# Kernel optimization log

Hardware: AMD Instinct MI355X
Metric: run time of the kernel (lower is better)

## Reference

```python
import jax, jax.numpy as jnp
import numpy as np

NUM_HEADS = 8
SPLIT_S = 4
DIM = 288            # n_feat * 3 * 3
SCALE = (DIM // NUM_HEADS) ** -0.5  # quirk: uses full dim's head_dim (36), not reduced
EPS = 1e-5


def _extract_patches(x):
    # x: [B,C,H,W] -> [B, C*9, H*W], 3x3 kernel, stride 1, 'same' padding
    B, C, H, W = x.shape
    xp = jnp.pad(x, ((0, 0), (0, 0), (1, 1), (1, 1)))
    pats = jnp.stack([xp[:, :, i:i + H, j:j + W] for i in range(3) for j in range(3)], axis=2)
    return pats.reshape(B, C * 9, H * W)


def _fold(cols, H, W):
    # inverse of extract: [B, C*9, H*W] -> [B,C,H,W], summing overlapping patches
    B, Ck, _ = cols.shape
    C = Ck // 9
    p = cols.reshape(B, C, 3, 3, H, W)
    out = jnp.zeros((B, C, H + 2, W + 2), cols.dtype)
    for i in range(3):
        for j in range(3):
            out = out.at[:, :, i:i + H, j:j + W].add(p[:, :, i, j])
    return out[:, :, 1:H + 1, 1:W + 1]


def _ln(x, w, b):
    mu = x.mean(-1, keepdims=True)
    var = ((x - mu) ** 2).mean(-1, keepdims=True)
    return (x - mu) * jax.lax.rsqrt(var + EPS) * w + b


def _attn(x, reduce_w, qkv_w, proj_w, proj_b):
    # x: [B,N,288] -> reduce -> [B,N,144] -> block-diag attention over s=4 chunks
    x = x @ reduce_w.T
    B, N, C = x.shape
    hd = C // NUM_HEADS
    qkv = (x @ qkv_w.T).reshape(B, N, 3, NUM_HEADS, hd).transpose(2, 0, 3, 1, 4)
    q, k, v = qkv[0], qkv[1], qkv[2]          # [B,h,N,hd]
    chunk = N // SPLIT_S
    q = q.reshape(B, NUM_HEADS, SPLIT_S, chunk, hd)
    k = k.reshape(B, NUM_HEADS, SPLIT_S, chunk, hd)
    v = v.reshape(B, NUM_HEADS, SPLIT_S, chunk, hd)
    attn = jnp.einsum('bhscd,bhsed->bhsce', q, k) * SCALE   # [B,h,s,chunk,chunk]
    attn = jax.nn.softmax(attn, axis=-1)
    out = jnp.einsum('bhsce,bhsed->bhscd', attn, v)          # [B,h,s,chunk,hd]
    out = out.transpose(0, 2, 3, 1, 4).reshape(B, N, C)      # cat chunks on token dim
    return out @ proj_w.T + proj_b


def setup_inputs() -> dict:
    key = jax.random.key(0)
    ks = jax.random.split(key, 12)
    d, dr, dh = DIM, DIM // 2, DIM // 4  # 288, 144, 72
    f = lambda k, shape: (jax.random.normal(k, shape, jnp.float32) * 0.02)
    return {
        'x': jax.random.normal(ks[0], (4, 32, 64, 64), jnp.float32),
        'ln1_w': jnp.ones((d,), jnp.float32), 'ln1_b': jnp.zeros((d,), jnp.float32),
        'reduce_w': f(ks[1], (dr, d)),
        'qkv_w': f(ks[2], (3 * dr, dr)),
        'proj_w': f(ks[3], (d, dr)), 'proj_b': jnp.zeros((d,), jnp.float32),
        'ln2_w': jnp.ones((d,), jnp.float32), 'ln2_b': jnp.zeros((d,), jnp.float32),
        'fc1_w': f(ks[4], (dh, d)), 'fc1_b': jnp.zeros((dh,), jnp.float32),
        'fc2_w': f(ks[5], (d, dh)), 'fc2_b': jnp.zeros((d,), jnp.float32),
    }


def reference(x, ln1_w, ln1_b, reduce_w, qkv_w, proj_w, proj_b, ln2_w, ln2_b, fc1_w, fc1_b, fc2_w, fc2_b):
    B, C, H, W = x.shape
    t = _extract_patches(x).transpose(0, 2, 1)  # [B, N=H*W, 288]
    t = t + _attn(_ln(t, ln1_w, ln1_b), reduce_w, qkv_w, proj_w, proj_b)
    h = _ln(t, ln2_w, ln2_b)
    t = t + (jax.nn.relu(h @ fc1_w.T + fc1_b) @ fc2_w.T + fc2_b)
    return _fold(t.transpose(0, 2, 1), H, W)
```

## Files before the change

kernel.cpp:

```cpp
#include <hip/hip_runtime.h>
#include <hip/hip_bf16.h>

typedef __hip_bfloat16 bf16;
typedef unsigned short u16;
typedef unsigned int u32;
typedef __attribute__((ext_vector_type(8))) short bf16x8;
typedef __attribute__((ext_vector_type(4))) float f32x4;

#define BB 4
#define CCH 32
#define HH 64
#define WW 64
#define NN 4096
#define D 288
#define DR 144
#define DQ 432
#define NH 8
#define HD 18
#define SPLIT 4
#define CHUNK 1024
#define DH 72
#define SCALE_ 0.16666666666666666f
#define QSCALE 0.24044917348149343f
#define EPS_ 1e-5f
#define ASTR 160
#define HSTR 96

__device__ __attribute__((aligned(16))) u16 g_Wcb[DQ * D];
__device__ __attribute__((aligned(16))) u16 g_pw[D * ASTR];
__device__ __attribute__((aligned(16))) u16 g_f1w[HSTR * D];
__device__ __attribute__((aligned(16))) u16 g_f2w[D * HSTR];
__device__ __attribute__((aligned(16))) u16 g_q[(size_t)BB * NH * NN * 32];
__device__ __attribute__((aligned(16))) u16 g_k[(size_t)BB * NH * NN * 32];
__device__ __attribute__((aligned(16))) u16 g_vt[(size_t)BB * NH * SPLIT * 32 * CHUNK];
__device__ __attribute__((aligned(16))) u16 g_attn[(size_t)BB * NN * ASTR];
__device__ __attribute__((aligned(16))) u16 g_h[(size_t)BB * NN * HSTR];
__device__ __attribute__((aligned(16))) u16 g_t0[(size_t)BB * NN * D];
__device__ __attribute__((aligned(16))) u16 g_t1[(size_t)BB * NN * D];
__device__ float g_t2[(size_t)BB * D * NN];
__device__ int   g_flag;

__device__ __forceinline__ float b2f(bf16 v) { return __bfloat162float(v); }
__device__ __forceinline__ float bits2f(u16 u) { return __uint_as_float(((u32)u) << 16); }
__device__ __forceinline__ u16 f2bits(float f) {
    u32 u = __float_as_uint(f);
    return (u16)((u + 0x7FFF + ((u >> 16) & 1)) >> 16);
}
__device__ __forceinline__ float ldin(const void* p, size_t i, int isbf) {
    return isbf ? b2f(((const bf16*)p)[i]) : ((const float*)p)[i];
}

#define RS  (D * ASTR + HSTR * D + D * HSTR)
#define RS2 (RS + BB * NH * SPLIT * CHUNK)
#define RSB ((RS2 + 255) / 256)
#define PATCHB (BB * HH)

__global__ void k_prep(const void* __restrict__ x, const void* __restrict__ qkv_w,
                       const void* __restrict__ reduce_w, const void* __restrict__ proj_w,
                       const void* __restrict__ fc1_w, const void* __restrict__ fc2_w) {
    __shared__ int cnt4[4];
    __shared__ float qw[DR];
    __shared__ float slab[32 * 3 * 66];
    int tid = threadIdx.x;
    {
        const u16* u = (const u16*)x;
        int c = 0;
        for (int i = tid; i < 2048; i += 256) c += (((u[i] >> 7) & 0xFF) >= 0x90);
        for (int o = 32; o; o >>= 1) c += __shfl_xor(c, o);
        if ((tid & 63) == 0) cnt4[tid >> 6] = c;
    }
    __syncthreads();
    int bf = (cnt4[0] + cnt4[1] + cnt4[2] + cnt4[3]) < 32;
    if (tid == 0 && blockIdx.x == 0) g_flag = bf;

    int bid = blockIdx.x;
    if (bid < DQ) {
        int o = bid;
        if (tid < DR) qw[tid] = ldin(qkv_w, (size_t)o * DR + tid, bf);
        __syncthreads();
        for (int col = tid; col < D; col += 256) {
            float s0 = 0.f, s1 = 0.f;
            #pragma unroll 4
            for (int j = 0; j < DR; j += 2) {
                s0 += qw[j] * ldin(reduce_w, (size_t)j * D + col, bf);
                s1 += qw[j + 1] * ldin(reduce_w, (size_t)(j + 1) * D + col, bf);
            }
            g_Wcb[(size_t)o * D + col] = f2bits(s0 + s1);
        }
    } else if (bid < DQ + RSB) {
        int idx = (bid - DQ) * 256 + tid;
        if (idx < D * ASTR) {
            int o = idx / ASTR, j = idx % ASTR;
            g_pw[idx] = (j < DR) ? f2bits(ldin(proj_w, (size_t)o * DR + j, bf)) : (u16)0;
        } else if (idx < D * ASTR + HSTR * D) {
            int t = idx - D * ASTR;
            int o = t / D;
            g_f1w[t] = (o < DH) ? f2bits(ldin(fc1_w, (size_t)t, bf)) : (u16)0;
        } else if (idx < RS) {
            int t = idx - D * ASTR - HSTR * D;
            int o = t / HSTR, j = t % HSTR;
            g_f2w[t] = (j < DH) ? f2bits(ldin(fc2_w, (size_t)o * DH + j, bf)) : (u16)0;
        } else if (idx < RS2) {
            int t = idx - RS;
            int bhs = t >> 10, n = t & 1023;
            g_vt[((size_t)bhs * 32 + 18) * CHUNK + n] = 0x3F80;
        }
    } else {
        int pb = bid - DQ - RSB;
        int b = pb >> 6, y = pb & 63;
        for (int idx = tid; idx < 32 * 3 * 66; idx += 256) {
            int c = idx / 198, rem = idx % 198;
            int ki = rem / 66, col = rem % 66 - 1;
            int sy = y + ki - 1;
            float v = 0.f;
            if (col >= 0 && col < 64 && sy >= 0 && sy < 64)
                v = ldin(x, ((size_t)(b * CCH + c) * HH + sy) * WW + col, bf);
            slab[idx] = v;
        }
        __syncthreads();
        size_t obase = ((size_t)b * NN + y * 64) * D;
        for (int idx = tid; idx < 64 * D; idx += 256) {
            int t = idx / D, f = idx % D;
            int c = f / 9, k = f % 9, ki = k / 3, kj = k % 3;
            g_t0[obase + idx] = f2bits(slab[c * 198 + ki * 66 + t + kj]);
        }
    }
}

__global__ void k_ln_qkv(const void* __restrict__ lnw, const void* __restrict__ lnb) {
    __shared__ __attribute__((aligned(16))) u16 xln[16 * 296];
    __shared__ float lnwf[D], lnbf[D];
    __shared__ float smu[16], srs[16];
    __shared__ u16 vbuf[144][18];
    int bf = g_flag;
    int tid = threadIdx.x;
    size_t tok0 = (size_t)blockIdx.x * 16;
    for (int i = tid; i < D; i += 256) { lnwf[i] = ldin(lnw, i, bf); lnbf[i] = ldin(lnb, i, bf); }
    {
        int tt = tid >> 4, p = tid & 15;
        const u32* pr = (const u32*)(g_t0 + (tok0 + tt) * D + p * 18);
        float s = 0.f, q = 0.f;
        #pragma unroll
        for (int j = 0; j < 9; ++j) {
            u32 v = pr[j];
            float a = bits2f((u16)(v & 0xFFFF)), b = bits2f((u16)(v >> 16));
            s += a + b; q += a * a + b * b;
        }
        #pragma unroll
        for (int o = 1; o < 16; o <<= 1) { s += __shfl_xor(s, o); q += __shfl_xor(q, o); }
        if (p == 0) {
            float mu = s / D;
            smu[tt] = mu;
            srs[tt] = rsqrtf(q / D - mu * mu + EPS_);
        }
    }
    __syncthreads();
    for (int idx = tid; idx < 16 * 144; idx += 256) {
        int t = idx / 144, dw = idx % 144;
        u32 v = *(const u32*)(g_t0 + (tok0 + t) * D + 2 * dw);
        float mu = smu[t], rs = srs[t];
        int f = 2 * dw;
        float a = (bits2f((u16)(v & 0xFFFF)) - mu) * rs * lnwf[f] + lnbf[f];
        float b = (bits2f((u16)(v >> 16)) - mu) * rs * lnwf[f + 1] + lnbf[f + 1];
        *(u32*)&xln[t * 296 + f] = (u32)f2bits(a) | ((u32)f2bits(b) << 16);
    }
    __syncthreads();
    int w = tid >> 6, lane = tid & 63, quad = lane >> 4, l15 = lane & 15;
    bf16x8 areg[9];
    const u16* abase = xln + l15 * 296 + quad * 8;
    #pragma unroll
    for (int ks = 0; ks < 9; ++ks) areg[ks] = *(const bf16x8*)(abase + ks * 32);
    int nt0 = w * 7, nt1 = (nt0 + 7 > 27) ? 27 : nt0 + 7;
    for (int nt = nt0; nt < nt1; ++nt) {
        f32x4 acc = {0.f, 0.f, 0.f, 0.f};
        const u16* bbase = g_Wcb + (size_t)(nt * 16 + l15) * D + quad * 8;
        #pragma unroll
        for (int ks = 0; ks < 9; ++ks) {
            bf16x8 bfr = *(const bf16x8*)(bbase + ks * 32);
            acc = __builtin_amdgcn_mfma_f32_16x16x32_bf16(areg[ks], bfr, acc, 0, 0, 0);
        }
        int o = nt * 16 + l15;
        int which = o / DR, rem = o % DR, hh = rem / HD, dd = rem % HD;
        #pragma unroll
        for (int r = 0; r < 4; ++r) {
            size_t token = tok0 + quad * 4 + r;
            int b_ = (int)(token >> 12), n = (int)(token & 4095);
            size_t row = (size_t)(b_ * NH + hh) * NN + n;
            if (which == 0)      g_q[row * 32 + dd] = f2bits(acc[r] * QSCALE);
            else if (which == 1) g_k[row * 32 + dd] = f2bits(acc[r]);
            else                 vbuf[rem][quad * 4 + r] = f2bits(acc[r]);
        }
    }
    __syncthreads();
    {
        int b_ = (int)(tok0 >> 12);
        int n0 = (int)(tok0 & 4095);
        int sIdx = n0 >> 10, nc = n0 & 1023;
        for (int idx = tid; idx < 144 * 16; idx += 256) {
            int rem = idx >> 4, t = idx & 15;
            int hh = rem / HD, dd = rem % HD;
            size_t voff = (((size_t)(b_ * NH + hh) * SPLIT + sIdx) * 32 + dd) * CHUNK + nc + t;
            g_vt[voff] = vbuf[rem][t];
        }
    }
}

#define PSTR 72
__global__ __launch_bounds__(128) void k_attn() {
    __shared__ __attribute__((aligned(16))) u16 Pl[2][4][16 * PSTR];
    int bid = blockIdx.x;
    int chunk = bid & 127, qblk = bid >> 7;
    int s = chunk & 3, bh = chunk >> 2;
    int tid = threadIdx.x;
    int w = tid >> 6, lane = tid & 63, quad = lane >> 4, l15 = lane & 15;

    size_t rowbase = (size_t)bh * NN + s * CHUNK;
    size_t vtbase = ((size_t)bh * SPLIT + s) * 32 * CHUNK;
    const u16* kbase = g_k + rowbase * 32 + quad * 8;
    const u16* vbase = g_vt + vtbase + quad * 8;

    int qbase = qblk * 128 + w * 64;
    bf16x8 qf[4];
    #pragma unroll
    for (int t = 0; t < 4; ++t)
        qf[t] = *(const bf16x8*)(g_q + (rowbase + qbase + t * 16 + l15) * 32 + quad * 8);

    f32x4 accA[4], accB[4];
    #pragma unroll
    for (int t = 0; t < 4; ++t) {
        accA[t] = (f32x4){0.f, 0.f, 0.f, 0.f};
        accB[t] = (f32x4){0.f, 0.f, 0.f, 0.f};
    }

    for (int kt = 0; kt < CHUNK; kt += 64) {
        bf16x8 kf0 = *(const bf16x8*)(kbase + (size_t)(kt + 2 * l15) * 32);
        bf16x8 kf1 = *(const bf16x8*)(kbase + (size_t)(kt + 2 * l15 + 1) * 32);
        bf16x8 kf2 = *(const bf16x8*)(kbase + (size_t)(kt + 32 + 2 * l15) * 32);
        bf16x8 kf3 = *(const bf16x8*)(kbase + (size_t)(kt + 33 + 2 * l15) * 32);
        bf16x8 vA0 = *(const bf16x8*)(vbase + (size_t)l15 * CHUNK + kt);
        bf16x8 vB0 = *(const bf16x8*)(vbase + (size_t)(16 + l15) * CHUNK + kt);
        bf16x8 vA1 = *(const bf16x8*)(vbase + (size_t)l15 * CHUNK + kt + 32);
        bf16x8 vB1 = *(const bf16x8*)(vbase + (size_t)(16 + l15) * CHUNK + kt + 32);
        f32x4 z = {0.f, 0.f, 0.f, 0.f};
        #pragma unroll
        for (int t = 0; t < 4; ++t) {
            u16* pw = Pl[w][t];
            f32x4 S0 = __builtin_amdgcn_mfma_f32_16x16x32_bf16(qf[t], kf0, z, 0, 0, 0);
            f32x4 S1 = __builtin_amdgcn_mfma_f32_16x16x32_bf16(qf[t], kf1, z, 0, 0, 0);
            f32x4 S2 = __builtin_amdgcn_mfma_f32_16x16x32_bf16(qf[t], kf2, z, 0, 0, 0);
            f32x4 S3 = __builtin_amdgcn_mfma_f32_16x16x32_bf16(qf[t], kf3, z, 0, 0, 0);
            #pragma unroll
            for (int r = 0; r < 4; ++r) {
                float p0 = exp2f(S0[r]), p1 = exp2f(S1[r]);
                float p2 = exp2f(S2[r]), p3 = exp2f(S3[r]);
                u32 w0 = __builtin_amdgcn_perm(__float_as_uint(p1), __float_as_uint(p0), 0x07060302u);
                u32 w1 = __builtin_amdgcn_perm(__float_as_uint(p3), __float_as_uint(p2), 0x07060302u);
                *(u32*)&pw[(quad * 4 + r) * PSTR + 2 * l15] = w0;
                *(u32*)&pw[(quad * 4 + r) * PSTR + 32 + 2 * l15] = w1;
            }
        }
        #pragma unroll
        for (int t = 0; t < 4; ++t) {
            const u16* pw = Pl[w][t];
            bf16x8 pf0 = *(const bf16x8*)&pw[l15 * PSTR + quad * 8];
            bf16x8 pf1 = *(const bf16x8*)&pw[l15 * PSTR + 32 + quad * 8];
            accA[t] = __builtin_amdgcn_mfma_f32_16x16x32_bf16(pf0, vA0, accA[t], 0, 0, 0);
            accB[t] = __builtin_amdgcn_mfma_f32_16x16x32_bf16(pf0, vB0, accB[t], 0, 0, 0);
            accA[t] = __builtin_amdgcn_mfma_f32_16x16x32_bf16(pf1, vA1, accA[t], 0, 0, 0);
            accB[t] = __builtin_amdgcn_mfma_f32_16x16x32_bf16(pf1, vB1, accB[t], 0, 0, 0);
        }
    }
    #pragma unroll
    for (int t = 0; t < 4; ++t) {
        #pragma unroll
        for (int r = 0; r < 4; ++r) {
            float lr = __shfl(accB[t][r], (lane & 48) | 2);
            float inv = 1.f / lr;
            int token = s * CHUNK + qbase + t * 16 + quad * 4 + r;
            size_t rowoff = ((size_t)(bh >> 3) * NN + token) * ASTR + (bh & 7) * HD;
            g_attn[rowoff + l15] = f2bits(accA[t][r] * inv);
            if (l15 < 2) g_attn[rowoff + 16 + l15] = f2bits(accB[t][r] * inv);
        }
    }
}

__global__ void k_proj_ln_fc1(const void* __restrict__ proj_b, const void* __restrict__ lnw,
                              const void* __restrict__ lnb, const void* __restrict__ fc1_b) {
    __shared__ float t1f[16][290];
    __shared__ __attribute__((aligned(16))) u16 xln[16 * 296];
    __shared__ float lnwf[D], lnbf[D];
    __shared__ float smu[16], srs[16];
    int bf = g_flag;
    int tid = threadIdx.x;
    size_t tok0 = (size_t)blockIdx.x * 16;
    int w = tid >> 6, lane = tid & 63, quad = lane >> 4, l15 = lane & 15;
    for (int i = tid; i < D; i += 256) { lnwf[i] = ldin(lnw, i, bf); lnbf[i] = ldin(lnb, i, bf); }

    {
        bf16x8 areg[5];
        const u16* abase = g_attn + (tok0 + l15) * ASTR + quad * 8;
        #pragma unroll
        for (int ks = 0; ks < 5; ++ks) areg[ks] = *(const bf16x8*)(abase + ks * 32);
        const int tab[5] = {0, 5, 10, 14, 18};
        for (int nt = tab[w]; nt < tab[w + 1]; ++nt) {
            f32x4 acc = {0.f, 0.f, 0.f, 0.f};
            const u16* bbase = g_pw + (size_t)(nt * 16 + l15) * ASTR + quad * 8;
            #pragma unroll
            for (int ks = 0; ks < 5; ++ks) {
                bf16x8 bfr = *(const bf16x8*)(bbase + ks * 32);
                acc = __builtin_amdgcn_mfma_f32_16x16x32_bf16(areg[ks], bfr, acc, 0, 0, 0);
            }
            int o = nt * 16 + l15;
            float bias = ldin(proj_b, o, bf);
            #pragma unroll
            for (int r = 0; r < 4; ++r) {
                size_t token = tok0 + quad * 4 + r;
                size_t off = token * D + o;
                float val = bits2f(g_t0[off]) + acc[r] + bias;
                g_t1[off] = f2bits(val);
                t1f[quad * 4 + r][o] = val;
            }
        }
    }
    __syncthreads();
    {
        int tt = tid >> 4, p = tid & 15;
        const float* src = &t1f[tt][p * 18];
        float s = 0.f, q = 0.f;
        #pragma unroll
        for (int j = 0; j < 18; ++j) { float a = src[j]; s += a; q += a * a; }
        #pragma unroll
        for (int o = 1; o < 16; o <<= 1) { s += __shfl_xor(s, o); q += __shfl_xor(q, o); }
        if (p == 0) {
            float mu = s / D;
            smu[tt] = mu;
            srs[tt] = rsqrtf(q / D - mu * mu + EPS_);
        }
    }
    __syncthreads();
    for (int idx = tid; idx < 16 * 144; idx += 256) {
        int t = idx / 144, dw = idx % 144;
        int f = 2 * dw;
        float mu = smu[t], rs = srs[t];
        float a = (t1f[t][f] - mu) * rs * lnwf[f] + lnbf[f];
        float b = (t1f[t][f + 1] - mu) * rs * lnwf[f + 1] + lnbf[f + 1];
        *(u32*)&xln[t * 296 + f] = (u32)f2bits(a) | ((u32)f2bits(b) << 16);
    }
    __syncthreads();
    {
        bf16x8 areg[9];
        const u16* abase = xln + l15 * 296 + quad * 8;
        #pragma unroll
        for (int ks = 0; ks < 9; ++ks) areg[ks] = *(const bf16x8*)(abase + ks * 32);
        const int tab2[5] = {0, 2, 4, 5, 6};
        for (int nt = tab2[w]; nt < tab2[w + 1]; ++nt) {
            f32x4 acc = {0.f, 0.f, 0.f, 0.f};
            const u16* bbase = g_f1w + (size_t)(nt * 16 + l15) * D + quad * 8;
            #pragma unroll
            for (int ks = 0; ks < 9; ++ks) {
                bf16x8 bfr = *(const bf16x8*)(bbase + ks * 32);
                acc = __builtin_amdgcn_mfma_f32_16x16x32_bf16(areg[ks], bfr, acc, 0, 0, 0);
            }
            int o = nt * 16 + l15;
            float bias = (o < DH) ? ldin(fc1_b, o, bf) : 0.f;
            #pragma unroll
            for (int r = 0; r < 4; ++r) {
                size_t token = tok0 + quad * 4 + r;
                g_h[token * HSTR + o] = f2bits(fmaxf(acc[r] + bias, 0.f));
            }
        }
    }
}

__global__ void k_fc2(const void* __restrict__ fc2_b) {
    __shared__ float t2f[16][293];
    int bf = g_flag;
    int tid = threadIdx.x;
    size_t tok0 = (size_t)blockIdx.x * 16;
    int w = tid >> 6, lane = tid & 63, quad = lane >> 4, l15 = lane & 15;
    bf16x8 areg[3];
    const u16* abase = g_h + (tok0 + l15) * HSTR + quad * 8;
    #pragma unroll
    for (int ks = 0; ks < 3; ++ks) areg[ks] = *(const bf16x8*)(abase + ks * 32);
    const int tab[5] = {0, 5, 10, 14, 18};
    for (int nt = tab[w]; nt < tab[w + 1]; ++nt) {
        f32x4 acc = {0.f, 0.f, 0.f, 0.f};
        const u16* bbase = g_f2w + (size_t)(nt * 16 + l15) * HSTR + quad * 8;
        #pragma unroll
        for (int ks = 0; ks < 3; ++ks) {
            bf16x8 bfr = *(const bf16x8*)(bbase + ks * 32);
            acc = __builtin_amdgcn_mfma_f32_16x16x32_bf16(areg[ks], bfr, acc, 0, 0, 0);
        }
        int o = nt * 16 + l15;
        float bias = ldin(fc2_b, o, bf);
        #pragma unroll
        for (int r = 0; r < 4; ++r) {
            size_t token = tok0 + quad * 4 + r;
            t2f[quad * 4 + r][o] = bits2f(g_t1[token * D + o]) + acc[r] + bias;
        }
    }
    __syncthreads();
    int b_ = (int)(tok0 >> 12), n0 = (int)(tok0 & 4095);
    for (int idx = tid; idx < D * 16; idx += 256) {
        int o = idx >> 4, t = idx & 15;
        g_t2[((size_t)b_ * D + o) * NN + n0 + t] = t2f[t][o];
    }
}

__global__ void k_fold(void* __restrict__ out) {
    int bf = g_flag;
    int idx = blockIdx.x * blockDim.x + threadIdx.x;
    if (idx >= BB * CCH * HH * WW) return;
    int xx = idx % WW;
    int y = (idx / WW) % HH;
    int c = (idx / (WW * HH)) % CCH;
    int b = idx / (WW * HH * CCH);
    const float* base = g_t2 + ((size_t)b * D + c * 9) * NN;
    float s = 0.f;
    #pragma unroll
    for (int i = 0; i < 3; ++i) {
        int sy = y + 1 - i;
        if (sy < 0 || sy >= HH) continue;
        #pragma unroll
        for (int j = 0; j < 3; ++j) {
            int sx = xx + 1 - j;
            if (sx < 0 || sx >= WW) continue;
            s += base[(size_t)(i * 3 + j) * NN + sy * WW + sx];
        }
    }
    if (bf) ((bf16*)out)[idx] = __float2bfloat16(s);
    else    ((float*)out)[idx] = s;
}

extern "C" void kernel_launch(void* const* d_in, const int* in_sizes, int n_in,
                              void* d_out, int out_size, void* d_ws, size_t ws_size,
                              hipStream_t stream) {
    const void* x        = d_in[0];
    const void* ln1_w    = d_in[1];
    const void* ln1_b    = d_in[2];
    const void* reduce_w = d_in[3];
    const void* qkv_w    = d_in[4];
    const void* proj_w   = d_in[5];
    const void* proj_b   = d_in[6];
    const void* ln2_w    = d_in[7];
    const void* ln2_b    = d_in[8];
    const void* fc1_w    = d_in[9];
    const void* fc1_b    = d_in[10];
    const void* fc2_w    = d_in[11];
    const void* fc2_b    = d_in[12];

    k_prep        <<<DQ + RSB + PATCHB, 256, 0, stream>>>(x, qkv_w, reduce_w, proj_w, fc1_w, fc2_w);
    k_ln_qkv      <<<BB * NN / 16, 256, 0, stream>>>(ln1_w, ln1_b);
    k_attn        <<<BB * NH * SPLIT * 8, 128, 0, stream>>>();
    k_proj_ln_fc1 <<<BB * NN / 16, 256, 0, stream>>>(proj_b, ln2_w, ln2_b, fc1_b);
    k_fc2         <<<BB * NN / 16, 256, 0, stream>>>(fc2_b);
    k_fold        <<<(BB * CCH * HH * WW + 255) / 256, 256, 0, stream>>>(d_out);
}
```

Measured before the change: 218.2 us.

## Split attention key dimension across two blocks and combine partials in new kernel

```diff
diff --git a/kernel.cpp b/kernel.cpp
--- a/kernel.cpp
+++ b/kernel.cpp
@@ -19,6 +19,7 @@
 #define HD 18
 #define SPLIT 4
 #define CHUNK 1024
+#define KS 512
 #define DH 72
 #define SCALE_ 0.16666666666666666f
 #define QSCALE 0.24044917348149343f
@@ -33,6 +34,7 @@
 __device__ __attribute__((aligned(16))) u16 g_q[(size_t)BB * NH * NN * 32];
 __device__ __attribute__((aligned(16))) u16 g_k[(size_t)BB * NH * NN * 32];
 __device__ __attribute__((aligned(16))) u16 g_vt[(size_t)BB * NH * SPLIT * 32 * CHUNK];
+__device__ __attribute__((aligned(16))) float g_part[2 * (size_t)BB * NH * NN * 20];
 __device__ __attribute__((aligned(16))) u16 g_attn[(size_t)BB * NN * ASTR];
 __device__ __attribute__((aligned(16))) u16 g_h[(size_t)BB * NN * HSTR];
 __device__ __attribute__((aligned(16))) u16 g_t0[(size_t)BB * NN * D];
@@ -209,7 +211,9 @@
 __global__ __launch_bounds__(128) void k_attn() {
     __shared__ __attribute__((aligned(16))) u16 Pl[2][4][16 * PSTR];
     int bid = blockIdx.x;
-    int chunk = bid & 127, qblk = bid >> 7;
+    int chunk = bid & 127;
+    int qblk = (bid >> 7) & 7;
+    int ksl = bid >> 10;
     int s = chunk & 3, bh = chunk >> 2;
     int tid = threadIdx.x;
     int w = tid >> 6, lane = tid & 63, quad = lane >> 4, l15 = lane & 15;
@@ -232,7 +236,9 @@
         accB[t] = (f32x4){0.f, 0.f, 0.f, 0.f};
     }
 
-    for (int kt = 0; kt < CHUNK; kt += 64) {
+    int kt0 = ksl * KS;
+    for (int kk = 0; kk < KS; kk += 64) {
+        int kt = kt0 + kk;
         bf16x8 kf0 = *(const bf16x8*)(kbase + (size_t)(kt + 2 * l15) * 32);
         bf16x8 kf1 = *(const bf16x8*)(kbase + (size_t)(kt + 2 * l15 + 1) * 32);
         bf16x8 kf2 = *(const bf16x8*)(kbase + (size_t)(kt + 32 + 2 * l15) * 32);
@@ -270,18 +276,33 @@
             accB[t] = __builtin_amdgcn_mfma_f32_16x16x32_bf16(pf1, vB1, accB[t], 0, 0, 0);
         }
     }
+    float* pb = g_part + (((size_t)ksl * 32 + bh) * SPLIT + s) * (size_t)(CHUNK * 20);
     #pragma unroll
     for (int t = 0; t < 4; ++t) {
         #pragma unroll
         for (int r = 0; r < 4; ++r) {
-            float lr = __shfl(accB[t][r], (lane & 48) | 2);
-            float inv = 1.f / lr;
-            int token = s * CHUNK + qbase + t * 16 + quad * 4 + r;
-            size_t rowoff = ((size_t)(bh >> 3) * NN + token) * ASTR + (bh & 7) * HD;
-            g_attn[rowoff + l15] = f2bits(accA[t][r] * inv);
-            if (l15 < 2) g_attn[rowoff + 16 + l15] = f2bits(accB[t][r] * inv);
-        }
-    }
+            int tokenc = qbase + t * 16 + quad * 4 + r;
+            float* row = pb + (size_t)tokenc * 20;
+            row[l15] = accA[t][r];
+            if (l15 < 3) row[16 + l15] = accB[t][r];
+        }
+    }
+}
+
+__global__ void k_comb() {
+    int bid = blockIdx.x;
+    int chunk = bid & 127, quarter = bid >> 7;
+    int s = chunk & 3, bh = chunk >> 2;
+    int b = bh >> 3, h = bh & 7;
+    int tokenc = quarter * 256 + threadIdx.x;
+    const float* p1 = g_part + (((size_t)bh) * SPLIT + s) * (size_t)(CHUNK * 20) + (size_t)tokenc * 20;
+    const float* p2 = p1 + (size_t)32 * SPLIT * CHUNK * 20;
+    float inv = 1.f / (p1[18] + p2[18]);
+    int token = s * CHUNK + tokenc;
+    size_t rowoff = ((size_t)b * NN + token) * ASTR + h * HD;
+    #pragma unroll
+    for (int d = 0; d < HD; ++d)
+        g_attn[rowoff + d] = f2bits((p1[d] + p2[d]) * inv);
 }
 
 __global__ void k_proj_ln_fc1(const void* __restrict__ proj_b, const void* __restrict__ lnw,
@@ -451,7 +472,8 @@
 
     k_prep        <<<DQ + RSB + PATCHB, 256, 0, stream>>>(x, qkv_w, reduce_w, proj_w, fc1_w, fc2_w);
     k_ln_qkv      <<<BB * NN / 16, 256, 0, stream>>>(ln1_w, ln1_b);
-    k_attn        <<<BB * NH * SPLIT * 8, 128, 0, stream>>>();
+    k_attn        <<<2 * BB * NH * SPLIT * 8, 128, 0, stream>>>();
+    k_comb        <<<BB * NH * SPLIT * 4, 256, 0, stream>>>();
     k_proj_ln_fc1 <<<BB * NN / 16, 256, 0, stream>>>(proj_b, ln2_w, ln2_b, fc1_b);
     k_fc2         <<<BB * NN / 16, 256, 0, stream>>>(fc2_b);
     k_fold        <<<(BB * CCH * HH * WW + 255) / 256, 256, 0, stream>>>(d_out);
```

New measurement: 227.0 us. +4.0%, slower.
